# Optimization experiments

Hardware: AMD Instinct MI355X
Metric: run time of the kernel (lower is better)

Reference implementation:

```python
import jax, jax.numpy as jnp
import numpy as np

N = 50000        # nodes
E = 800000       # edges (avg degree 16)
D_IN = 64
D_HID = 128      # 2 * out_dim
D_OUT = 64


def setup_inputs() -> dict:
    key = jax.random.key(0)
    ks = jax.random.split(key, 6)
    x = jax.random.normal(ks[0], (N, D_IN), dtype=jnp.float32)
    edge_index = jax.random.randint(ks[1], (2, E), 0, N, dtype=jnp.int32)
    # Glorot-style init like PyG GCNConv
    W1 = jax.random.normal(ks[2], (D_IN, D_HID), dtype=jnp.float32) / np.sqrt(D_IN)
    b1 = jnp.zeros((D_HID,), dtype=jnp.float32)
    W2 = jax.random.normal(ks[3], (D_HID, D_OUT), dtype=jnp.float32) / np.sqrt(D_HID)
    b2 = jnp.zeros((D_OUT,), dtype=jnp.float32)
    return {"x": x, "edge_index": edge_index, "W1": W1, "b1": b1, "W2": W2, "b2": b2}


def _gcn_norm(edge_index, num_nodes):
    # PyG GCNConv default: add self-loops, symmetric normalization D^-1/2 A_hat D^-1/2
    loop = jnp.arange(num_nodes, dtype=edge_index.dtype)
    src = jnp.concatenate([edge_index[0], loop])
    dst = jnp.concatenate([edge_index[1], loop])
    deg = jax.ops.segment_sum(jnp.ones_like(dst, dtype=jnp.float32), dst,
                              num_segments=num_nodes)
    dinv = jnp.where(deg > 0, jax.lax.rsqrt(deg), 0.0)
    norm = dinv[src] * dinv[dst]  # [E+N]
    return src, dst, norm


def _gcn_conv(x, W, b, src, dst, norm, num_nodes):
    h = x @ W                                      # [N, F_out]
    msg = h[src] * norm[:, None]                   # gather + scale, [E+N, F_out]
    out = jax.ops.segment_sum(msg, dst, num_segments=num_nodes)  # scatter-add
    return out + b


def reference(x, edge_index, W1, b1, W2, b2):
    num_nodes = x.shape[0]
    src, dst, norm = _gcn_norm(edge_index, num_nodes)
    h = _gcn_conv(x, W1, b1, src, dst, norm, num_nodes)
    h = jax.nn.relu(h)
    node_emb = _gcn_conv(h, W2, b2, src, dst, norm, num_nodes)
    return node_emb
```

## Files before the change

kernel.cpp:

```cpp
#include <hip/hip_runtime.h>

typedef unsigned short u16;
typedef unsigned int u32;

typedef __attribute__((ext_vector_type(8))) short bf16x8;
typedef __attribute__((ext_vector_type(4))) float f32x4;

#define BSH 8
#define CAP 5120
#define OVFCAP 8192
#define CHUNK 2048

__device__ __forceinline__ float bf2f(u16 u) {
    return __uint_as_float(((u32)u) << 16);
}
__device__ __forceinline__ u16 f2bf(float f) {
    u32 x = __float_as_uint(f);
    return (u16)((x + 0x7fffu + ((x >> 16) & 1u)) >> 16);
}

__device__ __forceinline__ bool block_isbf(const u16* __restrict__ x, float* sflag) {
    int tid = threadIdx.x;
    if (tid < 64) {
        u16 v = x[tid * 2];
        u32 ex = (v >> 7) & 0xFFu;
        unsigned long long m = __ballot(ex >= 90u && ex <= 140u);
        if (tid == 0) *sflag = (m == ~0ull) ? 1.0f : 0.0f;
    }
    __syncthreads();
    return *sflag != 0.0f;
}

__device__ __forceinline__ void acc8(uint4 w, float* a) {
    a[0] += bf2f((u16)(w.x & 0xFFFFu)); a[1] += bf2f((u16)(w.x >> 16));
    a[2] += bf2f((u16)(w.y & 0xFFFFu)); a[3] += bf2f((u16)(w.y >> 16));
    a[4] += bf2f((u16)(w.z & 0xFFFFu)); a[5] += bf2f((u16)(w.z >> 16));
    a[6] += bf2f((u16)(w.w & 0xFFFFu)); a[7] += bf2f((u16)(w.w >> 16));
}

__device__ __forceinline__ u32 scale2(u32 g, float di) {
    u16 lo = f2bf(bf2f((u16)(g & 0xFFFFu)) * di);
    u16 hi = f2bf(bf2f((u16)(g >> 16)) * di);
    return (u32)lo | ((u32)hi << 16);
}

__global__ __launch_bounds__(256) void k_binA2(
    const int* __restrict__ src, const int* __restrict__ dst,
    int* __restrict__ gcur, u32* __restrict__ staging,
    u32* __restrict__ ovf, int* __restrict__ ovfcur, int E) {
    __shared__ int hcnt[256];
    __shared__ int hbase[256];
    const int tid = threadIdx.x;
    const int e0 = blockIdx.x * CHUNK;
    const int e1 = min(e0 + CHUNK, E);
    hcnt[tid] = 0;
    __syncthreads();
    int dl[8], sl[8];
    const int eb = e0 + tid * 8;
    const bool vec = (eb + 7 < e1) &&
                     ((((size_t)(dst + eb)) | ((size_t)(src + eb))) & 15) == 0;
    if (vec) {
        int4 d0 = ((const int4*)(dst + eb))[0];
        int4 d1 = ((const int4*)(dst + eb))[1];
        int4 s0v = ((const int4*)(src + eb))[0];
        int4 s1v = ((const int4*)(src + eb))[1];
        dl[0] = d0.x; dl[1] = d0.y; dl[2] = d0.z; dl[3] = d0.w;
        dl[4] = d1.x; dl[5] = d1.y; dl[6] = d1.z; dl[7] = d1.w;
        sl[0] = s0v.x; sl[1] = s0v.y; sl[2] = s0v.z; sl[3] = s0v.w;
        sl[4] = s1v.x; sl[5] = s1v.y; sl[6] = s1v.z; sl[7] = s1v.w;
    } else {
#pragma unroll
        for (int k = 0; k < 8; k++) {
            int e = eb + k;
            bool ok = e < e1;
            dl[k] = ok ? dst[e] : -1;
            sl[k] = ok ? src[e] : 0;
        }
    }
#pragma unroll
    for (int k = 0; k < 8; k++)
        if (dl[k] >= 0) atomicAdd(&hcnt[dl[k] >> BSH], 1);
    __syncthreads();
    {
        int c = hcnt[tid];
        hbase[tid] = (c > 0) ? atomicAdd(&gcur[tid], c) : 0;
        hcnt[tid] = 0;
    }
    __syncthreads();
#pragma unroll
    for (int k = 0; k < 8; k++) {
        int d = dl[k];
        if (d < 0) continue;
        int b = d >> BSH;
        int r = atomicAdd(&hcnt[b], 1);
        int p = hbase[b] + r;
        if (p < CAP) {
            staging[(size_t)b * CAP + p] = (u32)sl[k] | ((u32)(d & 255) << 16);
        } else {
            int q = atomicAdd(ovfcur, 1);
            if (q < OVFCAP) ovf[q] = (u32)sl[k] | ((u32)d << 16);
        }
    }
}

__global__ __launch_bounds__(256) void k_bucket(
    const u32* __restrict__ staging, const int* __restrict__ gcur,
    const u32* __restrict__ ovf, const int* __restrict__ ovfcur,
    int* __restrict__ row_start, float* __restrict__ dinv,
    u16* __restrict__ csr, int nbuck,
    const void* __restrict__ W1, const void* __restrict__ b1,
    const void* __restrict__ W2, const void* __restrict__ b2,
    u16* __restrict__ wc,
    const void* __restrict__ x, u16* __restrict__ gxt, int N, int E) {
    __shared__ float sflag;
    __shared__ int hcnt[256];
    __shared__ int hscan[256];
    __shared__ int hcur[256];
    __shared__ int sred[256];
    __shared__ int sbase;
    __shared__ float sdinv[256];
    const int bid = blockIdx.x;
    const int tid = threadIdx.x;
    bool isbf = block_isbf((const u16*)x, &sflag);

    if (bid < nbuck) {
        const int b = bid;
        const int used = min(gcur[b], CAP);
        const u32* st = staging + (size_t)b * CAP;
        const int no = min(ovfcur[0], OVFCAP);
        const int used4 = used >> 2;
        sred[tid] = (tid < b) ? gcur[tid] : 0;
        hcnt[tid] = 0;
        __syncthreads();
        for (int s = 128; s > 0; s >>= 1) {
            if (tid < s) sred[tid] += sred[tid + s];
            __syncthreads();
        }
        if (tid == 0) sbase = sred[0];
        for (int i = tid; i < used4; i += 256) {
            uint4 p4 = ((const uint4*)st)[i];
            atomicAdd(&hcnt[p4.x >> 16], 1);
            atomicAdd(&hcnt[p4.y >> 16], 1);
            atomicAdd(&hcnt[p4.z >> 16], 1);
            atomicAdd(&hcnt[p4.w >> 16], 1);
        }
        for (int i = (used4 << 2) + tid; i < used; i += 256)
            atomicAdd(&hcnt[st[i] >> 16], 1);
        for (int i = tid; i < no; i += 256) {
            u32 pk = ovf[i];
            int d = (int)(pk >> 16);
            if ((d >> BSH) == b) atomicAdd(&hcnt[d & 255], 1);
        }
        __syncthreads();
        int v = hcnt[tid];
        hscan[tid] = v;
        __syncthreads();
        for (int s = 1; s < 256; s <<= 1) {
            int t = (tid >= s) ? hscan[tid - s] : 0;
            __syncthreads();
            hscan[tid] += t;
            __syncthreads();
        }
        int excl = hscan[tid] - v;
        hcur[tid] = excl;
        int base = sbase;
        float dv = rsqrtf((float)(v + 1));
        sdinv[tid] = dv;
        int node = (b << BSH) + tid;
        if (node < N) {
            row_start[node] = base + excl;
            dinv[node] = dv;
        }
        if (b == 0 && tid == 0) row_start[N] = E;
        __syncthreads();
        for (int i = tid; i < used4; i += 256) {
            uint4 p4 = ((const uint4*)st)[i];
            int r0 = atomicAdd(&hcur[p4.x >> 16], 1); csr[base + r0] = (u16)(p4.x & 0xFFFFu);
            int r1 = atomicAdd(&hcur[p4.y >> 16], 1); csr[base + r1] = (u16)(p4.y & 0xFFFFu);
            int r2 = atomicAdd(&hcur[p4.z >> 16], 1); csr[base + r2] = (u16)(p4.z & 0xFFFFu);
            int r3 = atomicAdd(&hcur[p4.w >> 16], 1); csr[base + r3] = (u16)(p4.w & 0xFFFFu);
        }
        for (int i = (used4 << 2) + tid; i < used; i += 256) {
            u32 pk = st[i];
            int r = atomicAdd(&hcur[pk >> 16], 1);
            csr[base + r] = (u16)(pk & 0xFFFFu);
        }
        for (int i = tid; i < no; i += 256) {
            u32 pk = ovf[i];
            int d = (int)(pk >> 16);
            if ((d >> BSH) == b) {
                int r = atomicAdd(&hcur[d & 255], 1);
                csr[base + r] = (u16)(pk & 0xFFFFu);
            }
        }
        const int row0 = b << BSH;
        for (int i = tid; i < 256 * 16; i += 256) {
            int rl = i >> 4;
            int node2 = row0 + rl;
            if (node2 >= N) break;
            int q = i & 15;
            size_t idx = (size_t)node2 * 16 + q;
            float di = sdinv[rl];
            float4 vv;
            if (isbf) {
                ushort4 u = ((const ushort4*)x)[idx];
                vv.x = bf2f(u.x); vv.y = bf2f(u.y); vv.z = bf2f(u.z); vv.w = bf2f(u.w);
            } else {
                vv = ((const float4*)x)[idx];
            }
            ushort4 o;
            o.x = f2bf(vv.x * di); o.y = f2bf(vv.y * di);
            o.z = f2bf(vv.z * di); o.w = f2bf(vv.w * di);
            ((ushort4*)gxt)[idx] = o;
        }
    } else {
        int cb = bid - nbuck;
        for (int i = cb * 256 + tid; i < 16576; i += 17 * 256) {
            const void* s; int off;
            if (i < 8192)       { int nn = i >> 6, k = i & 63;  s = W1; off = k * 128 + nn; }
            else if (i < 16384) { int j = i - 8192; int nn = j >> 7, k = j & 127; s = W2; off = k * 64 + nn; }
            else if (i < 16512) { s = b1; off = i - 16384; }
            else                { s = b2; off = i - 16512; }
            wc[i] = isbf ? ((const u16*)s)[off] : f2bf(((const float*)s)[off]);
        }
    }
}

template<bool FINAL>
__global__ __launch_bounds__(256) void k_gather(
    const uint4* __restrict__ feat, const int* __restrict__ row_start,
    const u16* __restrict__ csr, const float* __restrict__ dinv,
    const u16* __restrict__ b2c, const void* __restrict__ xdet,
    void* __restrict__ outp, int n) {
    __shared__ float sflag;
    bool isbf = true;
    if (FINAL) isbf = block_isbf((const u16*)xdet, &sflag);
    int t = blockIdx.x * 256 + threadIdx.x;
    int d = t >> 3;
    int lane = t & 7;
    if (d >= n) return;
    const uint4* fl = feat + lane;
    float a[8];
    {
        uint4 w = fl[(size_t)d * 8];
        a[0] = bf2f((u16)(w.x & 0xFFFFu)); a[1] = bf2f((u16)(w.x >> 16));
        a[2] = bf2f((u16)(w.y & 0xFFFFu)); a[3] = bf2f((u16)(w.y >> 16));
        a[4] = bf2f((u16)(w.z & 0xFFFFu)); a[5] = bf2f((u16)(w.z >> 16));
        a[6] = bf2f((u16)(w.w & 0xFFFFu)); a[7] = bf2f((u16)(w.w >> 16));
    }
    int s0 = row_start[d], s1 = row_start[d + 1];
    int j = s0;
    int cur = (j + lane < s1) ? (int)csr[j + lane] : 0;
    while (j + 8 <= s1) {
        int nxt = (j + 8 + lane < s1) ? (int)csr[j + 8 + lane] : 0;
        uint4 wv[8];
#pragma unroll
        for (int u = 0; u < 8; u++) {
            int sv = __shfl(cur, u, 8);
            wv[u] = fl[(size_t)sv * 8];
        }
#pragma unroll
        for (int u = 0; u < 8; u++) acc8(wv[u], a);
        cur = nxt;
        j += 8;
    }
    int rem = s1 - j;
    if (rem > 0) {
        for (int u = 0; u < rem; u++) {
            int sv = __shfl(cur, u, 8);
            uint4 wv = fl[(size_t)sv * 8];
            acc8(wv, a);
        }
    }
    if (FINAL) {
        float di = dinv[d];
#pragma unroll
        for (int u = 0; u < 8; u++)
            a[u] = a[u] * di + bf2f(b2c[8 * lane + u]);
        if (isbf) {
            uint4 o;
            o.x = (u32)f2bf(a[0]) | ((u32)f2bf(a[1]) << 16);
            o.y = (u32)f2bf(a[2]) | ((u32)f2bf(a[3]) << 16);
            o.z = (u32)f2bf(a[4]) | ((u32)f2bf(a[5]) << 16);
            o.w = (u32)f2bf(a[6]) | ((u32)f2bf(a[7]) << 16);
            ((uint4*)outp)[(size_t)d * 8 + lane] = o;
        } else {
            float4* op = (float4*)outp;
            op[(size_t)d * 16 + 2 * lane]     = make_float4(a[0], a[1], a[2], a[3]);
            op[(size_t)d * 16 + 2 * lane + 1] = make_float4(a[4], a[5], a[6], a[7]);
        }
    } else {
        uint4 o;
        o.x = (u32)f2bf(a[0]) | ((u32)f2bf(a[1]) << 16);
        o.y = (u32)f2bf(a[2]) | ((u32)f2bf(a[3]) << 16);
        o.z = (u32)f2bf(a[4]) | ((u32)f2bf(a[5]) << 16);
        o.w = (u32)f2bf(a[6]) | ((u32)f2bf(a[7]) << 16);
        ((uint4*)outp)[(size_t)d * 8 + lane] = o;
    }
}

__global__ __launch_bounds__(256) void k_mlp(
    const u16* __restrict__ accin, const u16* __restrict__ wc,
    const float* __restrict__ dinv, u16* outb, int n) {
    __shared__ __align__(16) u16 As[64 * 72];
    __shared__ __align__(16) u16 W1t[128 * 72];
    __shared__ __align__(16) u16 W2t[64 * 136];
    __shared__ __align__(16) u16 Hs[64 * 136];
    __shared__ float b1s[128];
    __shared__ float dvs[64];
    const int tid = threadIdx.x;
    const int row0 = blockIdx.x * 64;

    if (tid < 64) {
        int r = row0 + tid;
        dvs[tid] = (r < n) ? dinv[r] : 0.f;
    } else if (tid < 192) {
        b1s[tid - 64] = bf2f(wc[16384 + tid - 64]);
    }
    for (int i = tid; i < 512; i += 256) {
        int r = i >> 3, kk = i & 7;
        int row = row0 + r;
        uint4 v = make_uint4(0, 0, 0, 0);
        if (row < n) {
            uint4 g = ((const uint4*)accin)[(size_t)row * 8 + kk];
            float di = dinv[row];
            v.x = scale2(g.x, di); v.y = scale2(g.y, di);
            v.z = scale2(g.z, di); v.w = scale2(g.w, di);
        }
        *(uint4*)&As[r * 72 + kk * 8] = v;
    }
    for (int i = tid; i < 1024; i += 256) {
        int nn = i >> 3, kk = i & 7;
        *(uint4*)&W1t[nn * 72 + kk * 8] = ((const uint4*)wc)[i];
    }
    for (int i = tid; i < 1024; i += 256) {
        int nn = i >> 4, kk = i & 15;
        *(uint4*)&W2t[nn * 136 + kk * 8] = ((const uint4*)(wc + 8192))[i];
    }
    __syncthreads();

    const int wave = tid >> 6;
    const int lane = tid & 63;
    const int q = lane >> 4;
    const int ln = lane & 15;

    bf16x8 a[4][2];
#pragma unroll
    for (int mt = 0; mt < 4; mt++)
#pragma unroll
        for (int ks = 0; ks < 2; ks++)
            a[mt][ks] = *(const bf16x8*)&As[(mt * 16 + ln) * 72 + ks * 32 + q * 8];

    f32x4 c1[2][4];
#pragma unroll
    for (int ntl = 0; ntl < 2; ntl++)
#pragma unroll
        for (int mt = 0; mt < 4; mt++) c1[ntl][mt] = (f32x4){0.f, 0.f, 0.f, 0.f};

#pragma unroll
    for (int ntl = 0; ntl < 2; ntl++) {
        int nt = wave * 2 + ntl;
        bf16x8 b0 = *(const bf16x8*)&W1t[(nt * 16 + ln) * 72 + 0 + q * 8];
        bf16x8 b1f = *(const bf16x8*)&W1t[(nt * 16 + ln) * 72 + 32 + q * 8];
#pragma unroll
        for (int mt = 0; mt < 4; mt++) {
            c1[ntl][mt] = __builtin_amdgcn_mfma_f32_16x16x32_bf16(a[mt][0], b0, c1[ntl][mt], 0, 0, 0);
            c1[ntl][mt] = __builtin_amdgcn_mfma_f32_16x16x32_bf16(a[mt][1], b1f, c1[ntl][mt], 0, 0, 0);
        }
    }
#pragma unroll
    for (int ntl = 0; ntl < 2; ntl++) {
        int col = (wave * 2 + ntl) * 16 + ln;
        float bb = b1s[col];
#pragma unroll
        for (int mt = 0; mt < 4; mt++)
#pragma unroll
            for (int r = 0; r < 4; r++) {
                int hrow = mt * 16 + q * 4 + r;
                Hs[hrow * 136 + col] = f2bf(fmaxf(c1[ntl][mt][r] + bb, 0.f));
            }
    }
    __syncthreads();

    f32x4 c2[4];
#pragma unroll
    for (int mt = 0; mt < 4; mt++) c2[mt] = (f32x4){0.f, 0.f, 0.f, 0.f};
#pragma unroll
    for (int ks = 0; ks < 4; ks++) {
        bf16x8 bb = *(const bf16x8*)&W2t[(wave * 16 + ln) * 136 + ks * 32 + q * 8];
#pragma unroll
        for (int mt = 0; mt < 4; mt++) {
            bf16x8 aa = *(const bf16x8*)&Hs[(mt * 16 + ln) * 136 + ks * 32 + q * 8];
            c2[mt] = __builtin_amdgcn_mfma_f32_16x16x32_bf16(aa, bb, c2[mt], 0, 0, 0);
        }
    }
#pragma unroll
    for (int mt = 0; mt < 4; mt++)
#pragma unroll
        for (int r = 0; r < 4; r++) {
            int rloc = mt * 16 + q * 4 + r;
            int row = row0 + rloc;
            if (row < n) {
                int col = wave * 16 + ln;
                outb[(size_t)row * 64 + col] = f2bf(c2[mt][r] * dvs[rloc]);
            }
        }
}

extern "C" void kernel_launch(void* const* d_in, const int* in_sizes, int n_in,
                              void* d_out, int out_size, void* d_ws, size_t ws_size,
                              hipStream_t stream) {
    const void* x  = d_in[0];
    const int* ei  = (const int*)d_in[1];
    const void* W1 = d_in[2];
    const void* b1 = d_in[3];
    const void* W2 = d_in[4];
    const void* b2 = d_in[5];

    const int N = in_sizes[0] / 64;
    const int E = in_sizes[1] / 2;
    const int* src = ei;
    const int* dst = ei + E;

    float* ws = (float*)d_ws;
    const int NP = ((N + 64) + 63) & ~63;
    float* dinv    = ws;
    int* gcur      = (int*)(ws + NP);
    int* ovfcur    = gcur + 256;
    int* row_start = gcur + 320;
    u32* ovf       = (u32*)(row_start + ((N + 64) & ~63));
    u16* csr       = (u16*)(ovf + OVFCAP);
    u16* wc        = (u16*)(((size_t)(csr + E) + 255) & ~(size_t)255);
    u16* bufB      = (u16*)(((size_t)(wc + 16576) + 255) & ~(size_t)255);
    u32* staging   = (u32*)bufB;
    u16* gxt       = (u16*)d_out;

    const int gth = (N * 8 + 255) / 256;
    const int nbuck = (N + 255) >> BSH;
    const int binB = (E + CHUNK - 1) / CHUNK;
    dim3 blk(256);

    hipMemsetAsync(gcur, 0, 320 * sizeof(int), stream);
    k_binA2<<<dim3(binB), blk, 0, stream>>>(src, dst, gcur, staging, ovf, ovfcur, E);
    k_bucket<<<dim3(nbuck + 17), blk, 0, stream>>>(staging, gcur, ovf, ovfcur,
                                                   row_start, dinv, csr, nbuck,
                                                   W1, b1, W2, b2, wc, x, gxt, N, E);
    k_gather<false><<<dim3(gth), blk, 0, stream>>>((const uint4*)gxt, row_start, csr,
                                                   dinv, wc + 16512, x, bufB, N);
    k_mlp<<<dim3((N + 63) / 64), blk, 0, stream>>>((const u16*)bufB, wc, dinv, bufB, N);
    k_gather<true><<<dim3(gth), blk, 0, stream>>>((const uint4*)bufB, row_start, csr,
                                                  dinv, wc + 16512, x, d_out, N);
}
```

Measured before the change: 147.8 us.

## Fuse first-layer gather aggregation into the MLP kernel

Replaces the separate first-layer gather kernel and the MLP kernel with one kernel. Each 64-row block aggregates neighbour features straight into shared memory, scales them by dinv, then runs both MFMA matmuls. This removes one launch and the bf16 round trip of the aggregated features through global memory. It also aliases the W2 tile onto the A/W1 shared region, preloading W2 into registers, and raises wave priority around the MFMA loops. In exchange the irregular gather now runs inside a heavier kernel with more shared memory and register pressure, which may limit occupancy during the latency-bound gather.

```diff
diff --git a/kernel.cpp b/kernel.cpp
--- a/kernel.cpp
+++ b/kernel.cpp
@@ -36,12 +36,6 @@
     a[2] += bf2f((u16)(w.y & 0xFFFFu)); a[3] += bf2f((u16)(w.y >> 16));
     a[4] += bf2f((u16)(w.z & 0xFFFFu)); a[5] += bf2f((u16)(w.z >> 16));
     a[6] += bf2f((u16)(w.w & 0xFFFFu)); a[7] += bf2f((u16)(w.w >> 16));
-}
-
-__device__ __forceinline__ u32 scale2(u32 g, float di) {
-    u16 lo = f2bf(bf2f((u16)(g & 0xFFFFu)) * di);
-    u16 hi = f2bf(bf2f((u16)(g >> 16)) * di);
-    return (u32)lo | ((u32)hi << 16);
 }
 
 __global__ __launch_bounds__(256) void k_binA2(
@@ -299,44 +293,76 @@
     }
 }
 
-__global__ __launch_bounds__(256) void k_mlp(
-    const u16* __restrict__ accin, const u16* __restrict__ wc,
-    const float* __restrict__ dinv, u16* outb, int n) {
-    __shared__ __align__(16) u16 As[64 * 72];
-    __shared__ __align__(16) u16 W1t[128 * 72];
-    __shared__ __align__(16) u16 W2t[64 * 136];
+__global__ __launch_bounds__(256, 3) void k_gmlp(
+    const uint4* __restrict__ feat, const int* __restrict__ row_start,
+    const u16* __restrict__ csr, const float* __restrict__ dinv,
+    const u16* __restrict__ wc, u16* __restrict__ outb, int n) {
+    __shared__ __align__(16) u16 U[64 * 72 + 128 * 72];
     __shared__ __align__(16) u16 Hs[64 * 136];
     __shared__ float b1s[128];
     __shared__ float dvs[64];
+    u16* As  = U;
+    u16* W1t = U + 64 * 72;
+    u16* W2t = U;
+
     const int tid = threadIdx.x;
     const int row0 = blockIdx.x * 64;
 
+    for (int i = tid; i < 1024; i += 256) {
+        int nn = i >> 3, kk = i & 7;
+        *(uint4*)&W1t[nn * 72 + kk * 8] = ((const uint4*)wc)[i];
+    }
+    if (tid < 128) b1s[tid] = bf2f(wc[16384 + tid]);
     if (tid < 64) {
         int r = row0 + tid;
         dvs[tid] = (r < n) ? dinv[r] : 0.f;
-    } else if (tid < 192) {
-        b1s[tid - 64] = bf2f(wc[16384 + tid - 64]);
-    }
-    for (int i = tid; i < 512; i += 256) {
-        int r = i >> 3, kk = i & 7;
-        int row = row0 + r;
-        uint4 v = make_uint4(0, 0, 0, 0);
-        if (row < n) {
-            uint4 g = ((const uint4*)accin)[(size_t)row * 8 + kk];
-            float di = dinv[row];
-            v.x = scale2(g.x, di); v.y = scale2(g.y, di);
-            v.z = scale2(g.z, di); v.w = scale2(g.w, di);
-        }
-        *(uint4*)&As[r * 72 + kk * 8] = v;
-    }
-    for (int i = tid; i < 1024; i += 256) {
-        int nn = i >> 3, kk = i & 7;
-        *(uint4*)&W1t[nn * 72 + kk * 8] = ((const uint4*)wc)[i];
-    }
-    for (int i = tid; i < 1024; i += 256) {
-        int nn = i >> 4, kk = i & 15;
-        *(uint4*)&W2t[nn * 136 + kk * 8] = ((const uint4*)(wc + 8192))[i];
-    }
+    }
+
+    const int glane = tid & 7;
+    const uint4* fl = feat + glane;
+#pragma unroll
+    for (int half = 0; half < 2; half++) {
+        const int rloc = half * 32 + (tid >> 3);
+        const int d = row0 + rloc;
+        uint4 o = make_uint4(0, 0, 0, 0);
+        if (d < n) {
+            float a[8] = {0.f, 0.f, 0.f, 0.f, 0.f, 0.f, 0.f, 0.f};
+            acc8(fl[(size_t)d * 8], a);
+            int s0 = row_start[d], s1 = row_start[d + 1];
+            int j = s0;
+            int cur = (j + glane < s1) ? (int)csr[j + glane] : 0;
+            while (j + 8 <= s1) {
+                int nxt = (j + 8 + glane < s1) ? (int)csr[j + 8 + glane] : 0;
+                uint4 wv[8];
+#pragma unroll
+                for (int u = 0; u < 8; u++) {
+                    int sv = __shfl(cur, u, 8);
+                    wv[u] = fl[(size_t)sv * 8];
+                }
+#pragma unroll
+                for (int u = 0; u < 8; u++) acc8(wv[u], a);
+                cur = nxt;
+                j += 8;
+            }
+            int rem = s1 - j;
+            for (int u = 0; u < rem; u++) {
+                int sv = __shfl(cur, u, 8);
+                uint4 wv = fl[(size_t)sv * 8];
+                acc8(wv, a);
+            }
+            float di = dinv[d];
+            o.x = (u32)f2bf(a[0] * di) | ((u32)f2bf(a[1] * di) << 16);
+            o.y = (u32)f2bf(a[2] * di) | ((u32)f2bf(a[3] * di) << 16);
+            o.z = (u32)f2bf(a[4] * di) | ((u32)f2bf(a[5] * di) << 16);
+            o.w = (u32)f2bf(a[6] * di) | ((u32)f2bf(a[7] * di) << 16);
+        }
+        *(uint4*)&As[rloc * 72 + glane * 8] = o;
+    }
+
+    uint4 wreg[4];
+#pragma unroll
+    for (int u = 0; u < 4; u++) wreg[u] = ((const uint4*)(wc + 8192))[tid + 256 * u];
+
     __syncthreads();
 
     const int wave = tid >> 6;
@@ -357,6 +383,7 @@
 #pragma unroll
         for (int mt = 0; mt < 4; mt++) c1[ntl][mt] = (f32x4){0.f, 0.f, 0.f, 0.f};
 
+    __builtin_amdgcn_s_setprio(1);
 #pragma unroll
     for (int ntl = 0; ntl < 2; ntl++) {
         int nt = wave * 2 + ntl;
@@ -368,6 +395,7 @@
             c1[ntl][mt] = __builtin_amdgcn_mfma_f32_16x16x32_bf16(a[mt][1], b1f, c1[ntl][mt], 0, 0, 0);
         }
     }
+    __builtin_amdgcn_s_setprio(0);
 #pragma unroll
     for (int ntl = 0; ntl < 2; ntl++) {
         int col = (wave * 2 + ntl) * 16 + ln;
@@ -382,9 +410,18 @@
     }
     __syncthreads();
 
+#pragma unroll
+    for (int u = 0; u < 4; u++) {
+        int i = tid + 256 * u;
+        int nn = i >> 4, kk = i & 15;
+        *(uint4*)&W2t[nn * 136 + kk * 8] = wreg[u];
+    }
+    __syncthreads();
+
     f32x4 c2[4];
 #pragma unroll
     for (int mt = 0; mt < 4; mt++) c2[mt] = (f32x4){0.f, 0.f, 0.f, 0.f};
+    __builtin_amdgcn_s_setprio(1);
 #pragma unroll
     for (int ks = 0; ks < 4; ks++) {
         bf16x8 bb = *(const bf16x8*)&W2t[(wave * 16 + ln) * 136 + ks * 32 + q * 8];
@@ -394,6 +431,7 @@
             c2[mt] = __builtin_amdgcn_mfma_f32_16x16x32_bf16(aa, bb, c2[mt], 0, 0, 0);
         }
     }
+    __builtin_amdgcn_s_setprio(0);
 #pragma unroll
     for (int mt = 0; mt < 4; mt++)
 #pragma unroll
@@ -445,9 +483,8 @@
     k_bucket<<<dim3(nbuck + 17), blk, 0, stream>>>(staging, gcur, ovf, ovfcur,
                                                    row_start, dinv, csr, nbuck,
                                                    W1, b1, W2, b2, wc, x, gxt, N, E);
-    k_gather<false><<<dim3(gth), blk, 0, stream>>>((const uint4*)gxt, row_start, csr,
-                                                   dinv, wc + 16512, x, bufB, N);
-    k_mlp<<<dim3((N + 63) / 64), blk, 0, stream>>>((const u16*)bufB, wc, dinv, bufB, N);
+    k_gmlp<<<dim3((N + 63) / 64), blk, 0, stream>>>((const uint4*)gxt, row_start, csr,
+                                                    dinv, wc, bufB, N);
     k_gather<true><<<dim3(gth), blk, 0, stream>>>((const uint4*)bufB, row_start, csr,
                                                   dinv, wc + 16512, x, d_out, N);
 }
```

After: 160.1 us. 8.4% more time.
